# Kernel tuning notes

Hardware: AMD Instinct MI355X
Metric: run time of the kernel (lower is better)

Reference implementation:

```python
import jax, jax.numpy as jnp
import numpy as np

T, B, D, H = 512, 128, 1024, 1024


def setup_inputs() -> dict:
    key = jax.random.key(0)
    ks = jax.random.split(key, 9)
    s = 1.0 / np.sqrt(D + H)
    inputs = jax.random.normal(ks[0], (T, B, D), dtype=jnp.float32)
    Wf = jax.random.uniform(ks[1], (H, D + H), jnp.float32, -s, s)
    bf = jax.random.uniform(ks[2], (H,), jnp.float32, -s, s)
    Wi = jax.random.uniform(ks[3], (H, D + H), jnp.float32, -s, s)
    bi = jax.random.uniform(ks[4], (H,), jnp.float32, -s, s)
    Wg = jax.random.uniform(ks[5], (H, D + H), jnp.float32, -s, s)
    bg = jax.random.uniform(ks[6], (H,), jnp.float32, -s, s)
    Wo = jax.random.uniform(ks[7], (H, D + H), jnp.float32, -s, s)
    bo = jax.random.uniform(ks[8], (H,), jnp.float32, -s, s)
    return {"inputs": inputs, "Wf": Wf, "bf": bf, "Wi": Wi, "bi": bi,
            "Wg": Wg, "bg": bg, "Wo": Wo, "bo": bo}


def reference(inputs, Wf, bf, Wi, bi, Wg, bg, Wo, bo):
    # Classical LSTM cell, time-major inputs [T, B, D].
    batch = inputs.shape[1]
    h0 = jnp.zeros((batch, H), dtype=inputs.dtype)
    c0 = jnp.zeros((batch, H), dtype=inputs.dtype)

    def step(carry, x):
        h, c = carry
        combined = jnp.concatenate([x, h], axis=1)  # [B, D+H]
        f = jax.nn.sigmoid(combined @ Wf.T + bf)
        i = jax.nn.sigmoid(combined @ Wi.T + bi)
        g = jnp.tanh(combined @ Wg.T + bg)
        o = jax.nn.sigmoid(combined @ Wo.T + bo)
        c = f * c + i * g
        h = o * jnp.tanh(c)
        return (h, c), h

    (hT, cT), outputs = jax.lax.scan(step, (h0, c0), inputs)
    return outputs, (hT, cT)
```

## Files before the change

kernel.cpp:

```cpp
#include <hip/hip_runtime.h>


#define TT 512
#define BB 128

typedef __attribute__((ext_vector_type(8))) short short8;
typedef __attribute__((ext_vector_type(4))) float f32x4;

#define WX_OFF   0u
#define WH_OFF   8388608u
#define H_OFF    16777216u
#define C_OFF    17301504u
#define XBF_OFF  17825792u
#define ZX_OFF   51380224u
#define WS_MAIN  118489088u

__device__ __forceinline__ unsigned short f2bf(float x) {
    union { float f; unsigned int u; } a; a.f = x;
    unsigned int r = a.u + 0x7fff + ((a.u >> 16) & 1);
    return (unsigned short)(r >> 16);
}

__device__ __forceinline__ float fsig(float x) {
    float e = __expf(-x);
    return __builtin_amdgcn_rcpf(1.0f + e);
}
__device__ __forceinline__ float ftanh(float x) {
    float e = __expf(2.0f * x);
    return 1.0f - 2.0f * __builtin_amdgcn_rcpf(e + 1.0f);
}

__device__ __forceinline__ void gll16(const void* g, void* l) {
    __builtin_amdgcn_global_load_lds(
        (const __attribute__((address_space(1))) unsigned int*)g,
        (__attribute__((address_space(3))) unsigned int*)l, 16, 0, 0);
}


__global__ __launch_bounds__(256) void cvt_wi(const float* __restrict__ Wf,
                                              const float* __restrict__ Wi,
                                              const float* __restrict__ Wg,
                                              const float* __restrict__ Wo,
                                              unsigned short* __restrict__ Wxi,
                                              unsigned short* __restrict__ Whi) {
    const int n = blockIdx.x;
    const int k8 = threadIdx.x * 8;
    const int gate = n & 3, hcol = n >> 2;
    const float* src = ((gate == 0) ? Wf : (gate == 1) ? Wi : (gate == 2) ? Wg : Wo)
                       + (size_t)hcol * 2048 + k8;
    float4 a = *(const float4*)src;
    float4 b = *(const float4*)(src + 4);
    uint4 u;
    u.x = (unsigned)f2bf(a.x) | ((unsigned)f2bf(a.y) << 16);
    u.y = (unsigned)f2bf(a.z) | ((unsigned)f2bf(a.w) << 16);
    u.z = (unsigned)f2bf(b.x) | ((unsigned)f2bf(b.y) << 16);
    u.w = (unsigned)f2bf(b.z) | ((unsigned)f2bf(b.w) << 16);
    unsigned short* dst = (k8 < 1024) ? Wxi + (size_t)n * 1024 + k8
                                      : Whi + (size_t)n * 1024 + (k8 - 1024);
    *(uint4*)dst = u;
}

__global__ __launch_bounds__(256) void cvt_x(const float* __restrict__ X,
                                             unsigned short* __restrict__ dst) {
    size_t off = ((size_t)blockIdx.x * 256 + threadIdx.x) * 8;
    float4 a = *(const float4*)(X + off);
    float4 b = *(const float4*)(X + off + 4);
    uint4 u;
    u.x = (unsigned)f2bf(a.x) | ((unsigned)f2bf(a.y) << 16);
    u.y = (unsigned)f2bf(a.z) | ((unsigned)f2bf(a.w) << 16);
    u.z = (unsigned)f2bf(b.x) | ((unsigned)f2bf(b.y) << 16);
    u.w = (unsigned)f2bf(b.z) | ((unsigned)f2bf(b.w) << 16);
    *(uint4*)(dst + off) = u;
}

__global__ __launch_bounds__(256) void zero_ws(unsigned int* __restrict__ p) {
    p[blockIdx.x * 256 + threadIdx.x] = 0u;
}


__global__ __launch_bounds__(256) void gemm_zx128(
    const unsigned short* __restrict__ Xb,
    const unsigned short* __restrict__ Wxi,
    unsigned short* __restrict__ Zc) {
    __shared__ __align__(16) unsigned char smem[65536];

    const int tid = threadIdx.x;
    const int l = tid & 63;
    const int w = tid >> 6;
    const int wr = w >> 1, wc = w & 1;
    const int mt = blockIdx.x >> 5;
    const int nt = blockIdx.x & 31;
    const int lq = l >> 4, sp = l & 15;

    const int srow = l >> 3;
    const int sslot = l & 7;
    const unsigned short* As[4];
    const unsigned short* Bs[4];
    unsigned dstb[4];
#pragma unroll
    for (int q = 0; q < 4; ++q) {
        const int seg = w * 4 + q;
        const int row = seg * 8 + srow;
        const unsigned so = (unsigned)((sslot ^ (row & 7)) * 8);
        As[q] = Xb + (size_t)(mt * 128 + row) * 1024 + so;
        Bs[q] = Wxi + (size_t)(nt * 128 + row) * 1024 + so;
        dstb[q] = (unsigned)(seg * 1024);
    }

    auto stage = [&](int c, int buf) {
        unsigned char* Ab = smem + buf * 16384;
        unsigned char* Bb = smem + 32768 + buf * 16384;
#pragma unroll
        for (int q = 0; q < 4; ++q) {
            gll16(As[q] + c * 64, Ab + dstb[q]);
            gll16(Bs[q] + c * 64, Bb + dstb[q]);
        }
    };

    f32x4 acc[4][4];
#pragma unroll
    for (int m = 0; m < 4; ++m)
#pragma unroll
        for (int n = 0; n < 4; ++n) acc[m][n] = {0.f, 0.f, 0.f, 0.f};

    auto compute = [&](int buf) {
        const unsigned char* Ab = smem + buf * 16384;
        const unsigned char* Bb = smem + 32768 + buf * 16384;
        short8 af[4][2], bfr[4][2];
#pragma unroll
        for (int m = 0; m < 4; ++m) {
            const int ar = wr * 64 + m * 16 + sp;
            const unsigned abase = (unsigned)(ar * 128), axor = (unsigned)((ar & 7) << 4);
#pragma unroll
            for (int k2 = 0; k2 < 2; ++k2)
                af[m][k2] = *(const short8*)(Ab + abase +
                            (((unsigned)(k2 * 64 + lq * 16)) ^ axor));
        }
#pragma unroll
        for (int n = 0; n < 4; ++n) {
            const int br = wc * 64 + n * 16 + sp;
            const unsigned bbase = (unsigned)(br * 128), bxor = (unsigned)((br & 7) << 4);
#pragma unroll
            for (int k2 = 0; k2 < 2; ++k2)
                bfr[n][k2] = *(const short8*)(Bb + bbase +
                             (((unsigned)(k2 * 64 + lq * 16)) ^ bxor));
        }
#pragma unroll
        for (int m = 0; m < 4; ++m)
#pragma unroll
            for (int n = 0; n < 4; ++n) {
                acc[m][n] = __builtin_amdgcn_mfma_f32_16x16x32_bf16(
                    af[m][0], bfr[n][0], acc[m][n], 0, 0, 0);
                acc[m][n] = __builtin_amdgcn_mfma_f32_16x16x32_bf16(
                    af[m][1], bfr[n][1], acc[m][n], 0, 0, 0);
            }
    };

    stage(0, 0);
    __syncthreads();
    for (int c = 0; c < 16; ++c) {
        const int buf = c & 1;
        if (c < 15) stage(c + 1, buf ^ 1);
        compute(buf);
        __syncthreads();
    }

#pragma unroll
    for (int m = 0; m < 4; ++m) {
        const int ri = wr * 64 + m * 16 + lq * 4;
#pragma unroll
        for (int n = 0; n < 4; ++n) {
            const int ncol = nt * 128 + wc * 64 + n * 16 + sp;
            f32x4 z4 = acc[m][n];
            uint2 z2;
            z2.x = (unsigned)f2bf(z4[0]) | ((unsigned)f2bf(z4[1]) << 16);
            z2.y = (unsigned)f2bf(z4[2]) | ((unsigned)f2bf(z4[3]) << 16);
            *(uint2*)(Zc + (size_t)mt * 524288 + (size_t)(ri >> 2) * 16384 +
                      (size_t)ncol * 4) = z2;
        }
    }
}


__global__ __launch_bounds__(512) void lstm_step5(
    const unsigned short* __restrict__ Zslot,
    const unsigned short* __restrict__ Whi,
    const float* __restrict__ bfp, const float* __restrict__ bip,
    const float* __restrict__ bgp, const float* __restrict__ bop,
    const unsigned short* __restrict__ h_prev,
    unsigned short* __restrict__ h_next,
    float* __restrict__ c_ws,
    float* __restrict__ out, int t) {
    extern __shared__ __align__(16) unsigned char smem[];

    const int tid = threadIdx.x;
    const int l = tid & 63;
    const int w = tid >> 6;
    const int wm = w >> 1, wn = w & 1;
    const int rg = blockIdx.x >> 7;
    const int cg = blockIdx.x & 127;
    const int lq = l >> 4, sp = l & 15;
    const int g0 = l & 3;
    const int n = cg * 32 + wn * 16 + sp;
    const int j = n >> 2;
    const int j0 = cg * 8 + wn * 4;
    const int cidx = sp >> 2;
    const int srcb = l & 48;
    const int rbase = rg * 64 + wm * 16 + lq * 4;

    const float* bp = (g0 == 0) ? bfp : (g0 == 1) ? bip : (g0 == 2) ? bgp : bop;
    const float biasv = bp[j];
    uint2 zu = *(const uint2*)(Zslot + ((size_t)(rbase >> 2) * 4096 + n) * 4);
    float4 cp4 = *(const float4*)(c_ws + ((size_t)(rbase >> 2) * 1024 + j) * 4);

    f32x4 acc_a = {0.f, 0.f, 0.f, 0.f};
    f32x4 acc_b = {0.f, 0.f, 0.f, 0.f};

    const int ar0 = (w * 2 + 0) * 4 + (l >> 4);
    const int ar1 = (w * 2 + 1) * 4 + (l >> 4);
    const unsigned short* hsrc0 =
        h_prev + (size_t)(rg * 64 + ar0) * 1024 + ((sp ^ (ar0 & 7)) * 8);
    const unsigned short* hsrc1 =
        h_prev + (size_t)(rg * 64 + ar1) * 1024 + ((sp ^ (ar1 & 7)) * 8);
    const int brw = w * 4 + (l >> 4);
    const unsigned short* wsrc =
        Whi + (size_t)(cg * 32 + brw) * 1024 + ((sp ^ (brw & 7)) * 8);

    auto stage = [&](int c, int buf) {
        unsigned char* Ab = smem + buf * 16384;
        unsigned char* Bb = smem + 65536 + buf * 8192;
        gll16(hsrc0 + c * 128, Ab + (w * 2 + 0) * 1024);
        gll16(hsrc1 + c * 128, Ab + (w * 2 + 1) * 1024);
        gll16(wsrc + c * 128, Bb + w * 1024);
    };
    auto compute = [&](int buf) {
        const unsigned char* Ab = smem + buf * 16384;
        const unsigned char* Bb = smem + 65536 + buf * 8192;
        const int ar = wm * 16 + sp;
        const int br = wn * 16 + sp;
        const unsigned abase = (unsigned)(ar * 256), axor = (unsigned)((ar & 7) << 4);
        const unsigned bbase = (unsigned)(br * 256), bxor = (unsigned)((br & 7) << 4);
#pragma unroll
        for (int ks = 0; ks < 4; ++ks) {
            const unsigned kk2 = (unsigned)((ks * 4 + lq) << 4);
            short8 a = *(const short8*)(Ab + abase + (kk2 ^ axor));
            short8 b = *(const short8*)(Bb + bbase + (kk2 ^ bxor));
            if (ks & 1) acc_b = __builtin_amdgcn_mfma_f32_16x16x32_bf16(a, b, acc_b, 0, 0, 0);
            else        acc_a = __builtin_amdgcn_mfma_f32_16x16x32_bf16(a, b, acc_a, 0, 0, 0);
        }
    };

    stage(0, 0); stage(1, 1); stage(2, 2);

#define PH(c, WN, DO_STAGE)                                                   \
    asm volatile("s_waitcnt vmcnt(" #WN ") lgkmcnt(0)" ::: "memory");         \
    __builtin_amdgcn_sched_barrier(0);                                        \
    __builtin_amdgcn_s_barrier();                                             \
    if (DO_STAGE) stage((c) + 3, ((c) + 3) & 3);                              \
    compute((c) & 3);

    PH(0, 6, 1)
    PH(1, 6, 1)
    PH(2, 6, 1)
    PH(3, 6, 1)
    PH(4, 6, 1)
    PH(5, 6, 0)
    PH(6, 3, 0)
    PH(7, 0, 0)
#undef PH

    f32x4 z4 = acc_a + acc_b;
    z4[0] += __uint_as_float(zu.x << 16) + biasv;
    z4[1] += __uint_as_float(zu.x & 0xffff0000u) + biasv;
    z4[2] += __uint_as_float(zu.y << 16) + biasv;
    z4[3] += __uint_as_float(zu.y & 0xffff0000u) + biasv;
    float cpv[4] = {cp4.x, cp4.y, cp4.z, cp4.w};
    float hhv[4], ccv[4];
#pragma unroll
    for (int r = 0; r < 4; ++r) {
        float z = z4[r];
        float v1 = __shfl_xor(z, 1);
        float v2 = __shfl_xor(z, 2);
        float v3 = __shfl_xor(z, 3);
        float fg = fsig(z);
        float ig = fsig(v1);
        float gg = ftanh(v2);
        float og = fsig(v3);
        float cc = fg * cpv[r] + ig * gg;
        ccv[r] = cc;
        hhv[r] = og * ftanh(cc);
    }
    if (g0 == 0) {
        float4 q4; q4.x = ccv[0]; q4.y = ccv[1]; q4.z = ccv[2]; q4.w = ccv[3];
        *(float4*)(c_ws + ((size_t)(rbase >> 2) * 1024 + j) * 4) = q4;
    }
#pragma unroll
    for (int r = 0; r < 4; ++r) {
        float e0 = __shfl(hhv[r], srcb + 0);
        float e1 = __shfl(hhv[r], srcb + 4);
        float e2 = __shfl(hhv[r], srcb + 8);
        float e3 = __shfl(hhv[r], srcb + 12);
        if (g0 == 0 && cidx == r) {
            const int row = rbase + r;
            float4 o4; o4.x = e0; o4.y = e1; o4.z = e2; o4.w = e3;
            *(float4*)(&out[((size_t)t * BB + row) * 1024 + j0]) = o4;
            uint2 h2;
            h2.x = (unsigned)f2bf(e0) | ((unsigned)f2bf(e1) << 16);
            h2.y = (unsigned)f2bf(e2) | ((unsigned)f2bf(e3) << 16);
            *(uint2*)(&h_next[(size_t)row * 1024 + j0]) = h2;
        }
        if (t == TT - 1) {
            float d0 = __shfl(ccv[r], srcb + 0);
            float d1 = __shfl(ccv[r], srcb + 4);
            float d2 = __shfl(ccv[r], srcb + 8);
            float d3 = __shfl(ccv[r], srcb + 12);
            if (g0 == 0 && cidx == r) {
                const int row = rbase + r;
                float4 o4; o4.x = e0; o4.y = e1; o4.z = e2; o4.w = e3;
                float4 q4; q4.x = d0; q4.y = d1; q4.z = d2; q4.w = d3;
                *(float4*)(&out[(size_t)TT * BB * 1024 + (size_t)row * 1024 + j0]) = o4;
                *(float4*)(&out[(size_t)TT * BB * 1024 + (size_t)BB * 1024 +
                                (size_t)row * 1024 + j0]) = q4;
            }
        }
    }
}


__device__ __forceinline__ void gemm_tile_body(
    const float* __restrict__ Xt, const unsigned short* __restrict__ Wxi,
    unsigned short* __restrict__ Zslot, int mt, int cg, unsigned char* smem) {
    const int tid = threadIdx.x;
    const int l = tid & 63;
    const int w = tid >> 6;
    const int wr = w >> 1, wc = w & 1;
    const int lq = l >> 4, sp = l & 15;

    f32x4 acc_a = {0.f, 0.f, 0.f, 0.f};
    f32x4 acc_b = {0.f, 0.f, 0.f, 0.f};

    const int xrow = tid >> 3;
    const int xs = (tid & 7) * 2;
    const float* xsrc = Xt + (size_t)(mt * 32 + xrow) * 1024 + xs * 8;
    const unsigned xw0 = (unsigned)(xrow * 256 + ((xs * 16) ^ ((xrow & 7) << 4)));
    const unsigned xw1 = (unsigned)(xrow * 256 + (((xs + 1) * 16) ^ ((xrow & 7) << 4)));
    float4 xv0, xv1, xv2, xv3;

    const int bn0 = w * 8 + lq, bn1 = bn0 + 4;
    const unsigned short* wsrc0 = Wxi + (size_t)(cg * 32 + bn0) * 1024 + (sp ^ (bn0 & 7)) * 8;
    const unsigned short* wsrc1 = Wxi + (size_t)(cg * 32 + bn1) * 1024 + (sp ^ (bn1 & 7)) * 8;

    auto load_x = [&](int c) {
        const float* p = xsrc + c * 128;
        xv0 = *(const float4*)(p);     xv1 = *(const float4*)(p + 4);
        xv2 = *(const float4*)(p + 8); xv3 = *(const float4*)(p + 12);
    };
    auto write_x = [&](int buf) {
        unsigned char* Ab = smem + (buf ? 8192 : 0);
        uint4 u0, u1;
        u0.x = (unsigned)f2bf(xv0.x) | ((unsigned)f2bf(xv0.y) << 16);
        u0.y = (unsigned)f2bf(xv0.z) | ((unsigned)f2bf(xv0.w) << 16);
        u0.z = (unsigned)f2bf(xv1.x) | ((unsigned)f2bf(xv1.y) << 16);
        u0.w = (unsigned)f2bf(xv1.z) | ((unsigned)f2bf(xv1.w) << 16);
        u1.x = (unsigned)f2bf(xv2.x) | ((unsigned)f2bf(xv2.y) << 16);
        u1.y = (unsigned)f2bf(xv2.z) | ((unsigned)f2bf(xv2.w) << 16);
        u1.z = (unsigned)f2bf(xv3.x) | ((unsigned)f2bf(xv3.y) << 16);
        u1.w = (unsigned)f2bf(xv3.z) | ((unsigned)f2bf(xv3.w) << 16);
        *(uint4*)(Ab + xw0) = u0; *(uint4*)(Ab + xw1) = u1;
    };
    auto stage_B = [&](int c, int buf) {
        unsigned char* Bb = smem + 16384 + (buf ? 8192 : 0);
        gll16(wsrc0 + c * 128, Bb + (w * 8) * 256);
        gll16(wsrc1 + c * 128, Bb + (w * 8 + 4) * 256);
    };
    auto compute = [&](int buf) {
        const unsigned char* Ab = smem + (buf ? 8192 : 0);
        const unsigned char* Bb = smem + 16384 + (buf ? 8192 : 0);
        const int ar = wr * 16 + sp;
        const int br = wc * 16 + sp;
        const unsigned abase = (unsigned)(ar * 256), axor = (unsigned)((ar & 7) << 4);
        const unsigned bbase = (unsigned)(br * 256), bxor = (unsigned)((br & 7) << 4);
#pragma unroll
        for (int ks = 0; ks < 4; ++ks) {
            const unsigned kk2 = (unsigned)((ks * 4 + lq) << 4);
            short8 a = *(const short8*)(Ab + abase + (kk2 ^ axor));
            short8 b = *(const short8*)(Bb + bbase + (kk2 ^ bxor));
            if (ks & 1) acc_b = __builtin_amdgcn_mfma_f32_16x16x32_bf16(a, b, acc_b, 0, 0, 0);
            else        acc_a = __builtin_amdgcn_mfma_f32_16x16x32_bf16(a, b, acc_a, 0, 0, 0);
        }
    };

    load_x(0); stage_B(0, 0); write_x(0);
    __syncthreads();
    for (int c = 0; c < 8; ++c) {
        const int buf = c & 1, nbuf = buf ^ 1;
        if (c < 7) { load_x(c + 1); stage_B(c + 1, nbuf); }
        compute(buf);
        if (c < 7) write_x(nbuf);
        __syncthreads();
    }

    const int rowb = mt * 32 + wr * 16 + lq * 4;
    const int n = cg * 32 + wc * 16 + sp;
    f32x4 z4 = acc_a + acc_b;
    uint2 z2;
    z2.x = (unsigned)f2bf(z4[0]) | ((unsigned)f2bf(z4[1]) << 16);
    z2.y = (unsigned)f2bf(z4[2]) | ((unsigned)f2bf(z4[3]) << 16);
    *(uint2*)(Zslot + ((size_t)(rowb >> 2) * 4096 + n) * 4) = z2;
}

__global__ __launch_bounds__(256) void gemm_zx32(
    const float* __restrict__ X, const unsigned short* __restrict__ Wxi,
    unsigned short* __restrict__ Zring) {
    __shared__ __align__(16) unsigned char smem[32768];
    const int tl = blockIdx.x >> 9;
    const int inner = blockIdx.x & 511;
    gemm_tile_body(X + (size_t)tl * 131072, Wxi, Zring + (size_t)tl * 524288,
                   inner >> 7, inner & 127, smem);
}


extern "C" void kernel_launch(void* const* d_in, const int* in_sizes, int n_in,
                              void* d_out, int out_size, void* d_ws, size_t ws_size,
                              hipStream_t stream) {
    const float* X  = (const float*)d_in[0];
    const float* Wf = (const float*)d_in[1];
    const float* bf = (const float*)d_in[2];
    const float* Wi = (const float*)d_in[3];
    const float* bi = (const float*)d_in[4];
    const float* Wg = (const float*)d_in[5];
    const float* bg = (const float*)d_in[6];
    const float* Wo = (const float*)d_in[7];
    const float* bo = (const float*)d_in[8];
    unsigned char* ws = (unsigned char*)d_ws;

    unsigned short* Wxi = (unsigned short*)(ws + WX_OFF);
    unsigned short* Whi = (unsigned short*)(ws + WH_OFF);
    unsigned short* hbuf = (unsigned short*)(ws + H_OFF);
    float* c_ws = (float*)(ws + C_OFF);
    float* outp = (float*)d_out;

    cvt_wi<<<dim3(4096), dim3(256), 0, stream>>>(Wf, Wi, Wg, Wo, Wxi, Whi);
    zero_ws<<<dim3(1024), dim3(256), 0, stream>>>((unsigned int*)(ws + H_OFF));
    hipFuncSetAttribute((const void*)lstm_step5,
                        hipFuncAttributeMaxDynamicSharedMemorySize, 98304);

    if (ws_size >= WS_MAIN) {
        unsigned short* Xb = (unsigned short*)(ws + XBF_OFF);
        unsigned short* Zx = (unsigned short*)(ws + ZX_OFF);
        for (int q = 0; q < 4; ++q) {
            cvt_x<<<dim3(8192), dim3(256), 0, stream>>>(
                X + (size_t)q * 16777216, Xb);
            for (int c2 = 0; c2 < 2; ++c2) {
                gemm_zx128<<<dim3(2048), dim3(256), 0, stream>>>(
                    Xb + (size_t)c2 * 8388608, Wxi, Zx);
                for (int tl = 0; tl < 64; ++tl) {
                    const int t = q * 128 + c2 * 64 + tl;
                    const unsigned short* hp = hbuf + (size_t)(t & 1) * (BB * 1024);
                    unsigned short* hn = hbuf + (size_t)((t + 1) & 1) * (BB * 1024);
                    lstm_step5<<<dim3(256), dim3(512), 98304, stream>>>(
                        Zx + (size_t)tl * 524288, Whi, bf, bi, bg, bo,
                        hp, hn, c_ws, outp, t);
                }
            }
        }
    } else {
        unsigned short* Zx = (unsigned short*)(ws + XBF_OFF);
        int C = 4;
        const int cands[4] = {64, 16, 8, 4};
        for (int i = 0; i < 4; ++i) {
            if ((size_t)XBF_OFF + (size_t)cands[i] * 1048576u <= ws_size) { C = cands[i]; break; }
        }
        const int nchunks = TT / C;
        for (int ch = 0; ch < nchunks; ++ch) {
            gemm_zx32<<<dim3(C * 512), dim3(256), 0, stream>>>(
                X + (size_t)ch * C * 131072, Wxi, Zx);
            for (int tl = 0; tl < C; ++tl) {
                const int t = ch * C + tl;
                const unsigned short* hp = hbuf + (size_t)(t & 1) * (BB * 1024);
                unsigned short* hn = hbuf + (size_t)((t + 1) & 1) * (BB * 1024);
                lstm_step5<<<dim3(256), dim3(512), 98304, stream>>>(
                    Zx + (size_t)tl * 524288, Whi, bf, bi, bg, bo,
                    hp, hn, c_ws, outp, t);
            }
        }
    }
}
```

Baseline: 4.160 ms.

## Deepen GEMM pipeline and widen K chunks in LSTM step kernel

The input-projection GEMM moves to 512 threads, each wave owning a 32x64 subtile. Its double-buffered loop becomes a 4-stage cp.async-style pipeline with explicit vmcnt waits, and block indices are swizzled for better cache locality. The recurrent step kernel now loads K chunks of 256 instead of 128 into three buffers, cutting the phase and barrier count from 8 to 4. The cost is more shared memory per block (144KB and 128KB), which limits occupancy and leaves less slack in the pipelines.

```diff
diff --git a/kernel.cpp b/kernel.cpp
--- a/kernel.cpp
+++ b/kernel.cpp
@@ -78,58 +78,57 @@
 }
 
 
-__global__ __launch_bounds__(256) void gemm_zx128(
+__global__ __launch_bounds__(512) void gemm_zx128(
     const unsigned short* __restrict__ Xb,
     const unsigned short* __restrict__ Wxi,
     unsigned short* __restrict__ Zc) {
-    __shared__ __align__(16) unsigned char smem[65536];
+    extern __shared__ __align__(16) unsigned char smem[];
 
     const int tid = threadIdx.x;
     const int l = tid & 63;
     const int w = tid >> 6;
-    const int wr = w >> 1, wc = w & 1;
-    const int mt = blockIdx.x >> 5;
-    const int nt = blockIdx.x & 31;
+    const int wm = w >> 1, wn = w & 1;
+    const int swz = (int)((blockIdx.x & 7) * 256 + (blockIdx.x >> 3));
+    const int mt = swz >> 5;
+    const int nt = swz & 31;
     const int lq = l >> 4, sp = l & 15;
 
-    const int srow = l >> 3;
-    const int sslot = l & 7;
-    const unsigned short* As[4];
-    const unsigned short* Bs[4];
-    unsigned dstb[4];
-#pragma unroll
-    for (int q = 0; q < 4; ++q) {
-        const int seg = w * 4 + q;
-        const int row = seg * 8 + srow;
-        const unsigned so = (unsigned)((sslot ^ (row & 7)) * 8);
+    const unsigned short* As[2];
+    const unsigned short* Bs[2];
+    unsigned adst[2], bdst[2];
+#pragma unroll
+    for (int q = 0; q < 2; ++q) {
+        const int row = 16 * w + 8 * q + (l >> 3);
+        const unsigned so = (unsigned)(((l & 7) ^ (row & 7)) * 8);
         As[q] = Xb + (size_t)(mt * 128 + row) * 1024 + so;
         Bs[q] = Wxi + (size_t)(nt * 128 + row) * 1024 + so;
-        dstb[q] = (unsigned)(seg * 1024);
+        adst[q] = (unsigned)((16 * w + 8 * q) * 128);
+        bdst[q] = 65536u + adst[q];
     }
 
     auto stage = [&](int c, int buf) {
         unsigned char* Ab = smem + buf * 16384;
-        unsigned char* Bb = smem + 32768 + buf * 16384;
-#pragma unroll
-        for (int q = 0; q < 4; ++q) {
-            gll16(As[q] + c * 64, Ab + dstb[q]);
-            gll16(Bs[q] + c * 64, Bb + dstb[q]);
-        }
-    };
-
-    f32x4 acc[4][4];
-#pragma unroll
-    for (int m = 0; m < 4; ++m)
+        unsigned char* Bb = smem + buf * 16384;
+#pragma unroll
+        for (int q = 0; q < 2; ++q) {
+            gll16(As[q] + c * 64, Ab + adst[q]);
+            gll16(Bs[q] + c * 64, Bb + bdst[q]);
+        }
+    };
+
+    f32x4 acc[2][4];
+#pragma unroll
+    for (int m = 0; m < 2; ++m)
 #pragma unroll
         for (int n = 0; n < 4; ++n) acc[m][n] = {0.f, 0.f, 0.f, 0.f};
 
     auto compute = [&](int buf) {
         const unsigned char* Ab = smem + buf * 16384;
-        const unsigned char* Bb = smem + 32768 + buf * 16384;
-        short8 af[4][2], bfr[4][2];
-#pragma unroll
-        for (int m = 0; m < 4; ++m) {
-            const int ar = wr * 64 + m * 16 + sp;
+        const unsigned char* Bb = smem + 65536 + buf * 16384;
+        short8 af[2][2], bfr[4][2];
+#pragma unroll
+        for (int m = 0; m < 2; ++m) {
+            const int ar = wm * 32 + m * 16 + sp;
             const unsigned abase = (unsigned)(ar * 128), axor = (unsigned)((ar & 7) << 4);
 #pragma unroll
             for (int k2 = 0; k2 < 2; ++k2)
@@ -138,7 +137,7 @@
         }
 #pragma unroll
         for (int n = 0; n < 4; ++n) {
-            const int br = wc * 64 + n * 16 + sp;
+            const int br = wn * 64 + n * 16 + sp;
             const unsigned bbase = (unsigned)(br * 128), bxor = (unsigned)((br & 7) << 4);
 #pragma unroll
             for (int k2 = 0; k2 < 2; ++k2)
@@ -146,7 +145,7 @@
                              (((unsigned)(k2 * 64 + lq * 16)) ^ bxor));
         }
 #pragma unroll
-        for (int m = 0; m < 4; ++m)
+        for (int m = 0; m < 2; ++m)
 #pragma unroll
             for (int n = 0; n < 4; ++n) {
                 acc[m][n] = __builtin_amdgcn_mfma_f32_16x16x32_bf16(
@@ -156,21 +155,27 @@
             }
     };
 
-    stage(0, 0);
-    __syncthreads();
-    for (int c = 0; c < 16; ++c) {
-        const int buf = c & 1;
-        if (c < 15) stage(c + 1, buf ^ 1);
-        compute(buf);
-        __syncthreads();
-    }
-
-#pragma unroll
-    for (int m = 0; m < 4; ++m) {
-        const int ri = wr * 64 + m * 16 + lq * 4;
+    stage(0, 0); stage(1, 1); stage(2, 2);
+
+#define GPH(c, WN, DO_STAGE)                                                  \
+    asm volatile("s_waitcnt vmcnt(" #WN ") lgkmcnt(0)" ::: "memory");         \
+    __builtin_amdgcn_sched_barrier(0);                                        \
+    __builtin_amdgcn_s_barrier();                                             \
+    if (DO_STAGE) stage((c) + 3, ((c) + 3) & 3);                              \
+    compute((c) & 3);
+
+    GPH(0, 8, 1)  GPH(1, 8, 1)  GPH(2, 8, 1)  GPH(3, 8, 1)
+    GPH(4, 8, 1)  GPH(5, 8, 1)  GPH(6, 8, 1)  GPH(7, 8, 1)
+    GPH(8, 8, 1)  GPH(9, 8, 1)  GPH(10, 8, 1) GPH(11, 8, 1)
+    GPH(12, 8, 1) GPH(13, 8, 0) GPH(14, 4, 0) GPH(15, 0, 0)
+#undef GPH
+
+#pragma unroll
+    for (int m = 0; m < 2; ++m) {
+        const int ri = wm * 32 + m * 16 + lq * 4;
 #pragma unroll
         for (int n = 0; n < 4; ++n) {
-            const int ncol = nt * 128 + wc * 64 + n * 16 + sp;
+            const int ncol = nt * 128 + wn * 64 + n * 16 + sp;
             f32x4 z4 = acc[m][n];
             uint2 z2;
             z2.x = (unsigned)f2bf(z4[0]) | ((unsigned)f2bf(z4[1]) << 16);
@@ -182,7 +187,7 @@
 }
 
 
-__global__ __launch_bounds__(512) void lstm_step5(
+__global__ __launch_bounds__(512) void lstm_step6(
     const unsigned short* __restrict__ Zslot,
     const unsigned short* __restrict__ Whi,
     const float* __restrict__ bfp, const float* __restrict__ bip,
@@ -216,33 +221,43 @@
     f32x4 acc_a = {0.f, 0.f, 0.f, 0.f};
     f32x4 acc_b = {0.f, 0.f, 0.f, 0.f};
 
-    const int ar0 = (w * 2 + 0) * 4 + (l >> 4);
-    const int ar1 = (w * 2 + 1) * 4 + (l >> 4);
-    const unsigned short* hsrc0 =
-        h_prev + (size_t)(rg * 64 + ar0) * 1024 + ((sp ^ (ar0 & 7)) * 8);
-    const unsigned short* hsrc1 =
-        h_prev + (size_t)(rg * 64 + ar1) * 1024 + ((sp ^ (ar1 & 7)) * 8);
-    const int brw = w * 4 + (l >> 4);
-    const unsigned short* wsrc =
-        Whi + (size_t)(cg * 32 + brw) * 1024 + ((sp ^ (brw & 7)) * 8);
+    const unsigned short* As[4];
+    unsigned adst[4];
+#pragma unroll
+    for (int q = 0; q < 4; ++q) {
+        const int row = 8 * w + 2 * q + (l >> 5);
+        const unsigned so = (unsigned)(((l & 31) ^ (row & 7)) * 8);
+        As[q] = h_prev + (size_t)(rg * 64 + row) * 1024 + so;
+        adst[q] = (unsigned)((8 * w + 2 * q) * 512);
+    }
+    const unsigned short* Bs[2];
+    unsigned bdst[2];
+#pragma unroll
+    for (int e = 0; e < 2; ++e) {
+        const int row = 4 * w + 2 * e + (l >> 5);
+        const unsigned so = (unsigned)(((l & 31) ^ (row & 7)) * 8);
+        Bs[e] = Whi + (size_t)(cg * 32 + row) * 1024 + so;
+        bdst[e] = (unsigned)(98304 + (4 * w + 2 * e) * 512);
+    }
 
     auto stage = [&](int c, int buf) {
-        unsigned char* Ab = smem + buf * 16384;
-        unsigned char* Bb = smem + 65536 + buf * 8192;
-        gll16(hsrc0 + c * 128, Ab + (w * 2 + 0) * 1024);
-        gll16(hsrc1 + c * 128, Ab + (w * 2 + 1) * 1024);
-        gll16(wsrc + c * 128, Bb + w * 1024);
+        unsigned char* Ab = smem + buf * 32768;
+        unsigned char* Bb = smem + buf * 16384;
+#pragma unroll
+        for (int q = 0; q < 4; ++q) gll16(As[q] + c * 256, Ab + adst[q]);
+#pragma unroll
+        for (int e = 0; e < 2; ++e) gll16(Bs[e] + c * 256, Bb + bdst[e]);
     };
     auto compute = [&](int buf) {
-        const unsigned char* Ab = smem + buf * 16384;
-        const unsigned char* Bb = smem + 65536 + buf * 8192;
+        const unsigned char* Ab = smem + buf * 32768;
+        const unsigned char* Bb = smem + 98304 + buf * 16384;
         const int ar = wm * 16 + sp;
         const int br = wn * 16 + sp;
-        const unsigned abase = (unsigned)(ar * 256), axor = (unsigned)((ar & 7) << 4);
-        const unsigned bbase = (unsigned)(br * 256), bxor = (unsigned)((br & 7) << 4);
-#pragma unroll
-        for (int ks = 0; ks < 4; ++ks) {
-            const unsigned kk2 = (unsigned)((ks * 4 + lq) << 4);
+        const unsigned abase = (unsigned)(ar * 512), axor = (unsigned)((ar & 7) << 4);
+        const unsigned bbase = (unsigned)(br * 512), bxor = (unsigned)((br & 7) << 4);
+#pragma unroll
+        for (int ks = 0; ks < 8; ++ks) {
+            const unsigned kk2 = (unsigned)(ks * 64 + lq * 16);
             short8 a = *(const short8*)(Ab + abase + (kk2 ^ axor));
             short8 b = *(const short8*)(Bb + bbase + (kk2 ^ bxor));
             if (ks & 1) acc_b = __builtin_amdgcn_mfma_f32_16x16x32_bf16(a, b, acc_b, 0, 0, 0);
@@ -250,24 +265,19 @@
         }
     };
 
-    stage(0, 0); stage(1, 1); stage(2, 2);
-
-#define PH(c, WN, DO_STAGE)                                                   \
+    stage(0, 0); stage(1, 1);
+#define SPH(c, WN, DO_STAGE, SBUF)                                            \
     asm volatile("s_waitcnt vmcnt(" #WN ") lgkmcnt(0)" ::: "memory");         \
     __builtin_amdgcn_sched_barrier(0);                                        \
     __builtin_amdgcn_s_barrier();                                             \
-    if (DO_STAGE) stage((c) + 3, ((c) + 3) & 3);                              \
-    compute((c) & 3);
-
-    PH(0, 6, 1)
-    PH(1, 6, 1)
-    PH(2, 6, 1)
-    PH(3, 6, 1)
-    PH(4, 6, 1)
-    PH(5, 6, 0)
-    PH(6, 3, 0)
-    PH(7, 0, 0)
-#undef PH
+    if (DO_STAGE) stage((c) + 2, SBUF);                                       \
+    compute((c) % 3);
+
+    SPH(0, 6, 1, 2)
+    SPH(1, 6, 1, 0)
+    SPH(2, 6, 0, 0)
+    SPH(3, 0, 0, 0)
+#undef SPH
 
     f32x4 z4 = acc_a + acc_b;
     z4[0] += __uint_as_float(zu.x << 16) + biasv;
@@ -442,8 +452,10 @@
 
     cvt_wi<<<dim3(4096), dim3(256), 0, stream>>>(Wf, Wi, Wg, Wo, Wxi, Whi);
     zero_ws<<<dim3(1024), dim3(256), 0, stream>>>((unsigned int*)(ws + H_OFF));
-    hipFuncSetAttribute((const void*)lstm_step5,
-                        hipFuncAttributeMaxDynamicSharedMemorySize, 98304);
+    hipFuncSetAttribute((const void*)lstm_step6,
+                        hipFuncAttributeMaxDynamicSharedMemorySize, 147456);
+    hipFuncSetAttribute((const void*)gemm_zx128,
+                        hipFuncAttributeMaxDynamicSharedMemorySize, 131072);
 
     if (ws_size >= WS_MAIN) {
         unsigned short* Xb = (unsigned short*)(ws + XBF_OFF);
@@ -452,13 +464,13 @@
             cvt_x<<<dim3(8192), dim3(256), 0, stream>>>(
                 X + (size_t)q * 16777216, Xb);
             for (int c2 = 0; c2 < 2; ++c2) {
-                gemm_zx128<<<dim3(2048), dim3(256), 0, stream>>>(
+                gemm_zx128<<<dim3(2048), dim3(512), 131072, stream>>>(
                     Xb + (size_t)c2 * 8388608, Wxi, Zx);
                 for (int tl = 0; tl < 64; ++tl) {
                     const int t = q * 128 + c2 * 64 + tl;
                     const unsigned short* hp = hbuf + (size_t)(t & 1) * (BB * 1024);
                     unsigned short* hn = hbuf + (size_t)((t + 1) & 1) * (BB * 1024);
-                    lstm_step5<<<dim3(256), dim3(512), 98304, stream>>>(
+                    lstm_step6<<<dim3(256), dim3(512), 147456, stream>>>(
                         Zx + (size_t)tl * 524288, Whi, bf, bi, bg, bo,
                         hp, hn, c_ws, outp, t);
                 }
@@ -479,7 +491,7 @@
                 const int t = ch * C + tl;
                 const unsigned short* hp = hbuf + (size_t)(t & 1) * (BB * 1024);
                 unsigned short* hn = hbuf + (size_t)((t + 1) & 1) * (BB * 1024);
-                lstm_step5<<<dim3(256), dim3(512), 98304, stream>>>(
+                lstm_step6<<<dim3(256), dim3(512), 147456, stream>>>(
                     Zx + (size_t)tl * 524288, Whi, bf, bi, bg, bo,
                     hp, hn, c_ws, outp, t);
             }
```

New measurement: 4.389 ms. +5.5%, slower.
